# Optimization experiments

Measured on AMD Instinct MI355X. Metric: run time of the kernel, lower is better.

Reference implementation:

```python
import jax, jax.numpy as jnp
import numpy as np

B, L, D = 1, 2048, 2048
H, KVH, HD = 16, 4, 128
E, TOPK, G, TKG = 16, 4, 4, 2   # experts, top_k, n_group, topk_group
I, SH_I = 1024, 2048            # moe_intermediate, shared intermediate (1024*2)
EPS = 1e-5
THETA = 1e6
SCALE = HD ** -0.5
RSF = 2.5                        # routed_scaling_factor


def rms(x, w):
    return x * jax.lax.rsqrt(jnp.mean(x * x, axis=-1, keepdims=True) + EPS) * w


def rope(x):
    # x: [B, n_heads, L, HD], non-traditional (split-half) RoPE
    pos = jnp.arange(x.shape[2], dtype=jnp.float32)
    inv = 1.0 / (THETA ** (jnp.arange(0, HD, 2, dtype=jnp.float32) / HD))
    ang = pos[:, None] * inv[None, :]                    # [L, HD/2]
    cos, sin = jnp.cos(ang), jnp.sin(ang)
    x1, x2 = x[..., : HD // 2], x[..., HD // 2 :]
    return jnp.concatenate([x1 * cos - x2 * sin, x2 * cos + x1 * sin], axis=-1)


def setup_inputs() -> dict:
    key = jax.random.key(0)
    ks = jax.random.split(key, 13)
    s = 0.02
    mk = lambda k, shp: jax.random.normal(k, shp, jnp.float32) * s
    return {
        'x': jax.random.normal(ks[0], (B, L, D), jnp.float32),
        'w_q': mk(ks[1], (H * HD, D)),
        'w_k': mk(ks[2], (KVH * HD, D)),
        'w_v': mk(ks[3], (KVH * HD, D)),
        'w_o': mk(ks[4], (D, H * HD)),
        'q_norm_w': jnp.ones(HD, jnp.float32),
        'k_norm_w': jnp.ones(HD, jnp.float32),
        'ln1_w': jnp.ones(D, jnp.float32),
        'ln2_w': jnp.ones(D, jnp.float32),
        'gate_w': mk(ks[5], (E, D)),
        'gate_bias': mk(ks[6], (E,)),
        'wg': mk(ks[7], (E, I, D)),
        'wu': mk(ks[8], (E, I, D)),
        'wd': mk(ks[9], (E, D, I)),
        'sh_g': mk(ks[10], (SH_I, D)),
        'sh_u': mk(ks[11], (SH_I, D)),
        'sh_d': mk(ks[12], (D, SH_I)),
    }


def reference(x, w_q, w_k, w_v, w_o, q_norm_w, k_norm_w, ln1_w, ln2_w,
              gate_w, gate_bias, wg, wu, wd, sh_g, sh_u, sh_d):
    # ---- attention block ----
    h = rms(x, ln1_w)
    q = rms((h @ w_q.T).reshape(B, L, H, HD), q_norm_w).transpose(0, 2, 1, 3)
    k = rms((h @ w_k.T).reshape(B, L, KVH, HD), k_norm_w).transpose(0, 2, 1, 3)
    v = (h @ w_v.T).reshape(B, L, KVH, HD).transpose(0, 2, 1, 3)
    q, k = rope(q), rope(k)
    rep = H // KVH
    k = jnp.repeat(k, rep, axis=1)
    v = jnp.repeat(v, rep, axis=1)
    causal = jnp.tril(jnp.ones((L, L), bool))
    logits = jnp.einsum('bhqd,bhkd->bhqk', q, k) * SCALE
    logits = jnp.where(causal, logits, jnp.float32(-1e30))
    attn = jax.nn.softmax(logits, axis=-1)
    o = jnp.einsum('bhqk,bhkd->bhqd', attn, v).transpose(0, 2, 1, 3).reshape(B, L, H * HD)
    h1 = x + o @ w_o.T

    # ---- MoE block ----
    t = rms(h1, ln2_w).reshape(B * L, D)
    T = t.shape[0]
    # group-limited top-k gate (noaux_tc)
    sc = jax.nn.sigmoid(t @ gate_w.T)                    # [T, E] original scores
    s2 = sc + gate_bias
    sg = s2.reshape(T, G, E // G)
    group_scores = jax.lax.top_k(sg, 2)[0].sum(-1)       # [T, G]
    gidx = jax.lax.top_k(group_scores, TKG)[1]           # keep TKG best groups
    gmask = jnp.zeros((T, G), jnp.float32).at[jnp.arange(T)[:, None], gidx].set(1.0)
    masked = (sg * gmask[..., None]).reshape(T, E)       # dropped groups -> 0
    inds = jax.lax.top_k(masked, TOPK)[1]                # [T, TOPK]
    w = jnp.take_along_axis(sc, inds, axis=-1)
    w = w / (w.sum(-1, keepdims=True) + 1e-20) * RSF
    # combine weights scattered into [T, E]
    C = jnp.zeros((T, E), jnp.float32).at[jnp.arange(T)[:, None], inds].add(w)
    # expert SwiGLU (dense over experts, masked combine -> identical math)
    g = jnp.einsum('td,eid->tei', t, wg)
    u = jnp.einsum('td,eid->tei', t, wu)
    hm = jax.nn.silu(g) * u                               # [T, E, I]
    y = jnp.einsum('tei,edi,te->td', hm, wd, C)
    # shared experts
    sh = (jax.nn.silu(t @ sh_g.T) * (t @ sh_u.T)) @ sh_d.T
    return h1 + (y + sh).reshape(B, L, D)
```

## Files before the change

kernel.cpp:

```cpp
#include <hip/hip_runtime.h>
#include <math.h>

#define TT 2048
#define DM 2048
#define NHD 16
#define NKV 4
#define HDIM 128
#define NI 1024
#define ATT_SCALE 0.08838834764831845f

typedef unsigned short u16;
typedef __attribute__((ext_vector_type(8))) short short8;
typedef __attribute__((ext_vector_type(4))) short short4v;
typedef __attribute__((ext_vector_type(4))) float float4v;

#define AS1 __attribute__((address_space(1)))
#define AS3 __attribute__((address_space(3)))

__device__ __forceinline__ u16 f2bf(float f) {
  union { float f; unsigned u; } v; v.f = f;
  unsigned r = v.u + 0x7fffu + ((v.u >> 16) & 1u);
  return (u16)(r >> 16);
}
__device__ __forceinline__ float bf2f(u16 h) {
  union { unsigned u; float f; } v; v.u = ((unsigned)h) << 16;
  return v.f;
}
__device__ __forceinline__ float4v mfma16(short8 a, short8 b, float4v c) {
  return __builtin_amdgcn_mfma_f32_16x16x32_bf16(a, b, c, 0, 0, 0);
}
__device__ __forceinline__ void gl_lds(const u16* g, u16* l) {
  __builtin_amdgcn_global_load_lds((const AS1 void*)g, (AS3 void*)l, 16, 0, 0);
}

__global__ void cvt_split(const float* __restrict__ s, u16* __restrict__ oh,
                          u16* __restrict__ ol, int n) {
  int i = (blockIdx.x * 256 + threadIdx.x) * 4;
  if (i >= n) return;
  float4v v = *(const float4v*)(s + i);
  short4v vh, vl;
  #pragma unroll
  for (int c = 0; c < 4; ++c) {
    u16 hb = f2bf(v[c]);
    vh[c] = (short)hb;
    vl[c] = (short)f2bf(v[c] - bf2f(hb));
  }
  *(short4v*)(oh + i) = vh;
  *(short4v*)(ol + i) = vl;
}

__global__ void cvt_plain(const float* __restrict__ s, u16* __restrict__ o, int n) {
  int i = (blockIdx.x * 256 + threadIdx.x) * 8;
  if (i >= n) return;
  float4v v0 = *(const float4v*)(s + i);
  float4v v1 = *(const float4v*)(s + i + 4);
  short8 ov;
  #pragma unroll
  for (int c = 0; c < 4; ++c) {
    ov[c] = (short)f2bf(v0[c]);
    ov[c + 4] = (short)f2bf(v1[c]);
  }
  *(short8*)(o + i) = ov;
}

__global__ void rms_kernel(const float* __restrict__ in, const float* __restrict__ w,
                           u16* oh, u16* ol, float* of, u16* ob) {
  const int row = blockIdx.x, tid = threadIdx.x;
  const int lane = tid & 63, wvi = tid >> 6;
  const float* xr = in + (long)row * DM;
  float4v a = *(const float4v*)(xr + tid * 4);
  float4v b = *(const float4v*)(xr + 1024 + tid * 4);
  float ss = a[0]*a[0] + a[1]*a[1] + a[2]*a[2] + a[3]*a[3]
           + b[0]*b[0] + b[1]*b[1] + b[2]*b[2] + b[3]*b[3];
  #pragma unroll
  for (int m = 1; m < 64; m <<= 1) ss += __shfl_xor(ss, m);
  __shared__ float red[4];
  if (lane == 0) red[wvi] = ss;
  __syncthreads();
  float tot = red[0] + red[1] + red[2] + red[3];
  float sc = 1.0f / sqrtf(tot * (1.0f / 2048.0f) + 1e-5f);
  float4v w0 = *(const float4v*)(w + tid * 4);
  float4v w1 = *(const float4v*)(w + 1024 + tid * 4);
  #pragma unroll
  for (int c = 0; c < 4; ++c) {
    float v0 = a[c] * sc * w0[c];
    float v1 = b[c] * sc * w1[c];
    long i0 = (long)row * DM + tid * 4 + c;
    long i1 = i0 + 1024;
    if (oh) {
      u16 h0 = f2bf(v0); oh[i0] = h0; ol[i0] = f2bf(v0 - bf2f(h0));
      u16 h1 = f2bf(v1); oh[i1] = h1; ol[i1] = f2bf(v1 - bf2f(h1));
    }
    if (of) { of[i0] = v0; of[i1] = v1; }
    if (ob) { ob[i0] = f2bf(v0); ob[i1] = f2bf(v1); }
  }
}

__global__ void rope_kernel(const float* __restrict__ qlin, const float* __restrict__ klin,
                            const float* __restrict__ qw, const float* __restrict__ kw,
                            u16* qh, u16* ql, u16* kh, u16* kl) {
  int rw = blockIdx.x * 4 + (threadIdx.x >> 6);
  int lane = threadIdx.x & 63;
  int t = rw / 20, hh = rw - t * 20;
  const float* src; const float* nw; u16 *dh, *dl;
  if (hh < 16) {
    long ofs = (long)t * 2048 + hh * 128;
    src = qlin + ofs; nw = qw; dh = qh + ofs; dl = ql + ofs;
  } else {
    long ofs = (long)t * 512 + (hh - 16) * 128;
    src = klin + ofs; nw = kw; dh = kh + ofs; dl = kl + ofs;
  }
  float x1 = src[lane], x2 = src[lane + 64];
  float ss = x1 * x1 + x2 * x2;
  #pragma unroll
  for (int m = 1; m < 64; m <<= 1) ss += __shfl_xor(ss, m);
  float sc = 1.0f / sqrtf(ss * (1.0f / 128.0f) + 1e-5f);
  x1 *= sc * nw[lane];
  x2 *= sc * nw[lane + 64];
  double inv = pow(1.0e6, -(double)lane * (1.0 / 64.0));
  double ang = (double)t * inv;
  float cs = (float)cos(ang), sn = (float)sin(ang);
  float o1 = x1 * cs - x2 * sn;
  float o2 = x2 * cs + x1 * sn;
  u16 hb1 = f2bf(o1); dh[lane] = hb1;      dl[lane] = f2bf(o1 - bf2f(hb1));
  u16 hb2 = f2bf(o2); dh[lane + 64] = hb2; dl[lane + 64] = f2bf(o2 - bf2f(hb2));
}

struct GemmP {
  const u16* Ah; long aloOff;
  const u16* B0h; const u16* B1h; long blo0; long blo1; long bstride; int ns0;
  int K;
  const int* permA; const int* cnt; const int* offs;
  int fixedM; int maxRow;
  float* oF; int ldF;
  float* oF2; int ldF2; int osplit;
  u16* oB; long oBlo; int ldB;
  const float* addX;
  const u16* dslots; const int* inv;
};

template<int EPI, bool SPLIT>
__launch_bounds__(256, 2)
__global__ void gemm_bt(GemmP p) {
  const int e = blockIdx.z;
  const int cnt = p.cnt ? p.cnt[e] : p.fixedM;
  const int mt0 = blockIdx.x * 128;
  if (mt0 >= cnt) return;
  const int off = p.offs ? p.offs[e] : 0;
  const int nt0 = blockIdx.y * 128;

  __shared__ u16 lAh[128 * 64];
  __shared__ u16 lBh[128 * 64];
  __shared__ u16 lAl[SPLIT ? 128 * 64 : 8];
  __shared__ u16 lBl[SPLIT ? 128 * 64 : 8];

  const int tid = threadIdx.x;
  const int lane = tid & 63, wvi = tid >> 6;
  const int quad = lane >> 4, l16 = lane & 15;
  const int wm = (wvi >> 1) * 64, wn = (wvi & 1) * 64;
  const int srow = tid >> 3;
  const int scc = (tid & 7) ^ (srow & 7);

  const u16* agp[4];
  #pragma unroll
  for (int i = 0; i < 4; ++i) {
    int m = mt0 + i * 32 + srow;
    int r = off + m; if (r > p.maxRow) r = p.maxRow;
    if (p.permA) r = p.permA[r];
    agp[i] = p.Ah + (long)r * p.K + scc * 8;
  }
  const u16* bgph[4]; const u16* bgpl[4];
  #pragma unroll
  for (int j = 0; j < 4; ++j) {
    int n = nt0 + j * 32 + srow;
    const u16* bp; long lo;
    if (n < p.ns0) { bp = p.B0h + (long)e * p.bstride + (long)n * p.K; lo = p.blo0; }
    else           { bp = p.B1h + (long)e * p.bstride + (long)(n - p.ns0) * p.K; lo = p.blo1; }
    bgph[j] = bp + scc * 8;
    bgpl[j] = bp + lo + scc * 8;
  }

  float4v acc[4][4];
  #pragma unroll
  for (int a = 0; a < 4; ++a)
    #pragma unroll
    for (int b = 0; b < 4; ++b)
      acc[a][b] = (float4v){0.f, 0.f, 0.f, 0.f};

  const int wofs = wvi * 64 * 8;

  for (int k0 = 0; k0 < p.K; k0 += 64) {
    __syncthreads();
    #pragma unroll
    for (int i = 0; i < 4; ++i) {
      gl_lds(agp[i] + k0, &lAh[i * 2048 + wofs]);
      if constexpr (SPLIT) gl_lds(agp[i] + p.aloOff + k0, &lAl[i * 2048 + wofs]);
    }
    #pragma unroll
    for (int j = 0; j < 4; ++j) {
      gl_lds(bgph[j] + k0, &lBh[j * 2048 + wofs]);
      if constexpr (SPLIT) gl_lds(bgpl[j] + k0, &lBl[j * 2048 + wofs]);
    }
    __syncthreads();
    #pragma unroll
    for (int kc = 0; kc < 2; ++kc) {
      short8 ah[4], al[4], bh[4], bl[4];
      #pragma unroll
      for (int t = 0; t < 4; ++t) {
        int m = wm + t * 16 + l16;
        int ia = (m * 8 + ((kc * 4 + quad) ^ (m & 7))) * 8;
        ah[t] = *(const short8*)&lAh[ia];
        if constexpr (SPLIT) al[t] = *(const short8*)&lAl[ia];
        int n = wn + t * 16 + l16;
        int ib = (n * 8 + ((kc * 4 + quad) ^ (n & 7))) * 8;
        bh[t] = *(const short8*)&lBh[ib];
        if constexpr (SPLIT) bl[t] = *(const short8*)&lBl[ib];
      }
      #pragma unroll
      for (int mt = 0; mt < 4; ++mt)
        #pragma unroll
        for (int nt = 0; nt < 4; ++nt) {
          acc[mt][nt] = mfma16(ah[mt], bh[nt], acc[mt][nt]);
          if constexpr (SPLIT) {
            acc[mt][nt] = mfma16(ah[mt], bl[nt], acc[mt][nt]);
            acc[mt][nt] = mfma16(al[mt], bh[nt], acc[mt][nt]);
          }
        }
    }
  }

  #pragma unroll
  for (int mt = 0; mt < 4; ++mt) {
    #pragma unroll
    for (int nt = 0; nt < 4; ++nt) {
      const int n = nt0 + wn + nt * 16 + l16;
      const int mlb = wm + mt * 16 + quad * 4;
      if constexpr (EPI == 1) {
        short4v vh, vl;
        #pragma unroll
        for (int r = 0; r < 4; ++r) {
          float v = acc[mt][nt][r];
          u16 hb = f2bf(v);
          vh[r] = (short)hb;
          vl[r] = (short)f2bf(v - bf2f(hb));
        }
        long ix = (long)n * p.ldB + (mt0 + mlb);
        *(short4v*)&p.oB[ix] = vh;
        *(short4v*)&p.oB[ix + p.oBlo] = vl;
      } else {
        #pragma unroll
        for (int r = 0; r < 4; ++r) {
          const int gm = mt0 + mlb + r;
          if (gm >= cnt) continue;
          float v = acc[mt][nt][r];
          if constexpr (EPI == 0) {
            if (n < p.osplit) p.oF[(long)gm * p.ldF + n] = v;
            else p.oF2[(long)gm * p.ldF2 + (n - p.osplit)] = v;
          } else if constexpr (EPI == 2) {
            long ix = (long)gm * p.ldF + n;
            p.oF[ix] = v + p.addX[ix];
          } else if constexpr (EPI == 3) {
            p.oB[(long)(off + gm) * p.ldB + n] = f2bf(v);
          } else if constexpr (EPI == 5) {
            long ix = (long)gm * p.ldF + n;
            const int* iv = p.inv + gm * 4;
            float s = bf2f(p.dslots[(long)iv[0] * DM + n])
                    + bf2f(p.dslots[(long)iv[1] * DM + n])
                    + bf2f(p.dslots[(long)iv[2] * DM + n])
                    + bf2f(p.dslots[(long)iv[3] * DM + n]);
            p.oF[ix] = v + p.addX[ix] + s;
          }
        }
      }
    }
  }
}

__launch_bounds__(256, 2)
__global__ void attn_kernel(const u16* __restrict__ qh, const u16* __restrict__ ql,
                            const u16* __restrict__ kh, const u16* __restrict__ kl,
                            const u16* __restrict__ vh, const u16* __restrict__ vl,
                            u16* __restrict__ oh, u16* __restrict__ ol) {
  const int head = blockIdx.x;
  const int qt = (int)gridDim.y - 1 - blockIdx.y;
  const int kvh = head >> 2;
  const int tid = threadIdx.x;
  const int lane = tid & 63, wvi = tid >> 6;
  const int quad = lane >> 4, l16 = lane & 15;

  __shared__ u16 lKh[64 * 128];
  __shared__ u16 lKl[64 * 128];
  __shared__ u16 lVh[128 * 64];
  __shared__ u16 lVl[128 * 64];

  const int qbase = qt * 128;
  short8 qfh[2][4], qfl[2][4];
  #pragma unroll
  for (int mt = 0; mt < 2; ++mt) {
    int row = qbase + wvi * 32 + mt * 16 + l16;
    const u16* ph = qh + (long)row * (NHD * HDIM) + head * HDIM + quad * 8;
    const u16* pl = ql + (long)row * (NHD * HDIM) + head * HDIM + quad * 8;
    #pragma unroll
    for (int kc = 0; kc < 4; ++kc) {
      qfh[mt][kc] = *(const short8*)(ph + kc * 32);
      qfl[mt][kc] = *(const short8*)(pl + kc * 32);
    }
  }
  float4v oacc[2][8];
  #pragma unroll
  for (int mt = 0; mt < 2; ++mt)
    #pragma unroll
    for (int dt = 0; dt < 8; ++dt)
      oacc[mt][dt] = (float4v){0.f, 0.f, 0.f, 0.f};
  float mrun[2][4], lrun[2][4];
  #pragma unroll
  for (int mt = 0; mt < 2; ++mt)
    #pragma unroll
    for (int r = 0; r < 4; ++r) { mrun[mt][r] = -INFINITY; lrun[mt][r] = 0.f; }

  const int sck = (tid & 15) ^ (tid >> 4);
  const int scv = (tid & 7) ^ ((tid >> 3) & 7);
  const int nsteps = 2 * qt + 2;

  for (int kt = 0; kt < nsteps; ++kt) {
    const int t0 = kt * 64;
    __syncthreads();
    #pragma unroll
    for (int i = 0; i < 4; ++i) {
      int krow = i * 16 + (tid >> 4);
      long kg = (long)(t0 + krow) * (NKV * HDIM) + kvh * HDIM + sck * 8;
      gl_lds(kh + kg, &lKh[(i * 256 + wvi * 64) * 8]);
      gl_lds(kl + kg, &lKl[(i * 256 + wvi * 64) * 8]);
      int vrow = i * 32 + (tid >> 3);
      long vg = (long)(kvh * HDIM + vrow) * TT + t0 + scv * 8;
      gl_lds(vh + vg, &lVh[(i * 256 + wvi * 64) * 8]);
      gl_lds(vl + vg, &lVl[(i * 256 + wvi * 64) * 8]);
    }
    __syncthreads();

    float4v s[2][4];
    #pragma unroll
    for (int mt = 0; mt < 2; ++mt)
      #pragma unroll
      for (int nt = 0; nt < 4; ++nt)
        s[mt][nt] = (float4v){0.f, 0.f, 0.f, 0.f};
    #pragma unroll
    for (int kc = 0; kc < 4; ++kc) {
      #pragma unroll
      for (int nt = 0; nt < 4; ++nt) {
        int n = nt * 16 + l16;
        int idx = (n * 16 + ((kc * 4 + quad) ^ (n & 15))) * 8;
        short8 bh = *(const short8*)&lKh[idx];
        short8 bl = *(const short8*)&lKl[idx];
        #pragma unroll
        for (int mt = 0; mt < 2; ++mt) {
          s[mt][nt] = mfma16(qfh[mt][kc], bh, s[mt][nt]);
          s[mt][nt] = mfma16(qfh[mt][kc], bl, s[mt][nt]);
          s[mt][nt] = mfma16(qfl[mt][kc], bh, s[mt][nt]);
        }
      }
    }
    const bool dg = (kt >= 2 * qt);
    #pragma unroll
    for (int mt = 0; mt < 2; ++mt)
      #pragma unroll
      for (int nt = 0; nt < 4; ++nt)
        #pragma unroll
        for (int r = 0; r < 4; ++r) {
          float v = s[mt][nt][r] * ATT_SCALE;
          if (dg) {
            int kcol = t0 + nt * 16 + l16;
            int qrow = qbase + wvi * 32 + mt * 16 + quad * 4 + r;
            if (kcol > qrow) v = -1e30f;
          }
          s[mt][nt][r] = v;
        }
    float alf[2][4];
    #pragma unroll
    for (int mt = 0; mt < 2; ++mt)
      #pragma unroll
      for (int r = 0; r < 4; ++r) {
        float mx = fmaxf(fmaxf(s[mt][0][r], s[mt][1][r]), fmaxf(s[mt][2][r], s[mt][3][r]));
        mx = fmaxf(mx, __shfl_xor(mx, 1));
        mx = fmaxf(mx, __shfl_xor(mx, 2));
        mx = fmaxf(mx, __shfl_xor(mx, 4));
        mx = fmaxf(mx, __shfl_xor(mx, 8));
        float mnew = fmaxf(mrun[mt][r], mx);
        float al = expf(mrun[mt][r] - mnew);
        float ps = 0.f;
        #pragma unroll
        for (int nt = 0; nt < 4; ++nt) {
          float pv = expf(s[mt][nt][r] - mnew);
          s[mt][nt][r] = pv;
          ps += pv;
        }
        ps += __shfl_xor(ps, 1); ps += __shfl_xor(ps, 2);
        ps += __shfl_xor(ps, 4); ps += __shfl_xor(ps, 8);
        lrun[mt][r] = lrun[mt][r] * al + ps;
        mrun[mt][r] = mnew;
        alf[mt][r] = al;
      }
    #pragma unroll
    for (int mt = 0; mt < 2; ++mt)
      #pragma unroll
      for (int dt = 0; dt < 8; ++dt)
        #pragma unroll
        for (int r = 0; r < 4; ++r)
          oacc[mt][dt][r] *= alf[mt][r];
    __syncthreads();
    #pragma unroll
    for (int mt = 0; mt < 2; ++mt)
      #pragma unroll
      for (int nt = 0; nt < 4; ++nt)
        #pragma unroll
        for (int r = 0; r < 4; ++r) {
          int row = wvi * 32 + mt * 16 + quad * 4 + r;
          int col = nt * 16 + l16;
          int idx = (row * 8 + ((col >> 3) ^ (row & 7))) * 8 + (col & 7);
          float pv = s[mt][nt][r];
          u16 hb = f2bf(pv);
          lKh[idx] = hb;
          lKl[idx] = f2bf(pv - bf2f(hb));
        }
    __syncthreads();
    #pragma unroll
    for (int kc = 0; kc < 2; ++kc) {
      short8 ph[2], pl[2];
      #pragma unroll
      for (int mt = 0; mt < 2; ++mt) {
        int m = wvi * 32 + mt * 16 + l16;
        int idx = (m * 8 + ((kc * 4 + quad) ^ (m & 7))) * 8;
        ph[mt] = *(const short8*)&lKh[idx];
        pl[mt] = *(const short8*)&lKl[idx];
      }
      #pragma unroll
      for (int dt = 0; dt < 8; ++dt) {
        int d = dt * 16 + l16;
        int idx = (d * 8 + ((kc * 4 + quad) ^ (d & 7))) * 8;
        short8 wh = *(const short8*)&lVh[idx];
        short8 wl = *(const short8*)&lVl[idx];
        #pragma unroll
        for (int mt = 0; mt < 2; ++mt) {
          oacc[mt][dt] = mfma16(ph[mt], wh, oacc[mt][dt]);
          oacc[mt][dt] = mfma16(ph[mt], wl, oacc[mt][dt]);
          oacc[mt][dt] = mfma16(pl[mt], wh, oacc[mt][dt]);
        }
      }
    }
  }
  #pragma unroll
  for (int mt = 0; mt < 2; ++mt)
    #pragma unroll
    for (int dt = 0; dt < 8; ++dt)
      #pragma unroll
      for (int r = 0; r < 4; ++r) {
        int row = qbase + wvi * 32 + mt * 16 + quad * 4 + r;
        int d = dt * 16 + l16;
        float v = oacc[mt][dt][r] / lrun[mt][r];
        long ix = (long)row * (NHD * HDIM) + head * HDIM + d;
        u16 hb = f2bf(v);
        oh[ix] = hb;
        ol[ix] = f2bf(v - bf2f(hb));
      }
}

__global__ void routing_kernel(const float* __restrict__ t32, const float* __restrict__ gw,
                               const float* __restrict__ gb,
                               int* inds, float* wv, int* counts) {
  int t = blockIdx.x;
  int lane = threadIdx.x;
  const float* tr = t32 + (long)t * DM;
  float4v tv[8];
  #pragma unroll
  for (int j = 0; j < 8; ++j) tv[j] = *(const float4v*)(tr + lane * 32 + j * 4);
  float sc[16];
  for (int e = 0; e < 16; ++e) {
    const float* g = gw + (long)e * DM + lane * 32;
    float acc = 0.f;
    #pragma unroll
    for (int j = 0; j < 8; ++j) {
      float4v gv = *(const float4v*)(g + j * 4);
      acc += tv[j][0]*gv[0] + tv[j][1]*gv[1] + tv[j][2]*gv[2] + tv[j][3]*gv[3];
    }
    #pragma unroll
    for (int m = 1; m < 64; m <<= 1) acc += __shfl_xor(acc, m);
    sc[e] = 1.f / (1.f + expf(-acc));
  }
  if (lane == 0) {
    float s2[16];
    for (int e = 0; e < 16; ++e) s2[e] = sc[e] + gb[e];
    float gs[4];
    for (int g = 0; g < 4; ++g) {
      float xq[4] = { s2[4*g], s2[4*g+1], s2[4*g+2], s2[4*g+3] };
      int am = 0; float m1 = xq[0];
      for (int i = 1; i < 4; ++i) if (xq[i] > m1) { m1 = xq[i]; am = i; }
      float m2 = -1e30f;
      for (int i = 0; i < 4; ++i) if (i != am) m2 = fmaxf(m2, xq[i]);
      gs[g] = m1 + m2;
    }
    int g0 = 0;
    for (int g = 1; g < 4; ++g) if (gs[g] > gs[g0]) g0 = g;
    int g1 = -1;
    for (int g = 0; g < 4; ++g) if (g != g0 && (g1 < 0 || gs[g] > gs[g1])) g1 = g;
    float msk[16];
    for (int e = 0; e < 16; ++e) {
      int g = e >> 2;
      msk[e] = (g == g0 || g == g1) ? s2[e] : 0.0f;
    }
    int id[4]; float w[4]; float wsum = 0.f;
    for (int j = 0; j < 4; ++j) {
      int bi = 0; float bv = msk[0];
      for (int e = 1; e < 16; ++e) if (msk[e] > bv) { bv = msk[e]; bi = e; }
      id[j] = bi; w[j] = sc[bi]; msk[bi] = -1e30f;
      wsum += w[j];
    }
    float scale = 2.5f / (wsum + 1e-20f);
    for (int j = 0; j < 4; ++j) {
      inds[t * 4 + j] = id[j];
      wv[t * 4 + j] = w[j] * scale;
      atomicAdd(&counts[id[j]], 1);
    }
  }
}

__global__ void scan_kernel(int* ctrl) {
  if (threadIdx.x == 0) {
    int a = 0;
    for (int e = 0; e < 16; ++e) { ctrl[16 + e] = a; a += ctrl[e]; }
  }
}

__global__ void assign_kernel(const int* inds, const float* wv, int* ctrl,
                              int* perm, float* wslot, int* inv) {
  int t = blockIdx.x * 256 + threadIdx.x;
  if (t >= TT) return;
  for (int j = 0; j < 4; ++j) {
    int e = inds[t * 4 + j];
    int pos = atomicAdd(&ctrl[32 + e], 1);
    int s = ctrl[16 + e] + pos;
    perm[s] = t;
    wslot[s] = wv[t * 4 + j];
    inv[t * 4 + j] = s;
  }
}

__global__ void hm_moe_kernel(const u16* __restrict__ gu, const float* __restrict__ wslot,
                              u16* __restrict__ hm) {
  int slot = blockIdx.x;
  int i = threadIdx.x * 4;
  float w = wslot[slot];
  const u16* gp = gu + (long)slot * 2048;
  short4v gv = *(const short4v*)(gp + i);
  short4v uv = *(const short4v*)(gp + 1024 + i);
  short4v ov;
  #pragma unroll
  for (int c = 0; c < 4; ++c) {
    float g = bf2f((u16)gv[c]);
    float u = bf2f((u16)uv[c]);
    float h = g / (1.f + expf(-g)) * u * w;
    ov[c] = (short)f2bf(h);
  }
  *(short4v*)&hm[(long)slot * 1024 + i] = ov;
}

__global__ void hm_sh_kernel(const u16* __restrict__ gu, u16* __restrict__ hm) {
  int t = blockIdx.x;
  int i = threadIdx.x * 8;
  const u16* gp = gu + (long)t * 4096 + i;
  const u16* up = gu + (long)t * 4096 + 2048 + i;
  u16* op = hm + (long)t * 2048 + i;
  #pragma unroll
  for (int c = 0; c < 2; ++c) {
    short4v gv = *(const short4v*)(gp + c * 4);
    short4v uv = *(const short4v*)(up + c * 4);
    short4v ov;
    #pragma unroll
    for (int q = 0; q < 4; ++q) {
      float g = bf2f((u16)gv[q]);
      float u = bf2f((u16)uv[q]);
      float h = g / (1.f + expf(-g)) * u;
      ov[q] = (short)f2bf(h);
    }
    *(short4v*)(op + c * 4) = ov;
  }
}

extern "C" void kernel_launch(void* const* d_in, const int* in_sizes, int n_in,
                              void* d_out, int out_size, void* d_ws, size_t ws_size,
                              hipStream_t stream) {
  (void)in_sizes; (void)n_in; (void)out_size; (void)ws_size;
  const float* x   = (const float*)d_in[0];
  const float* wq  = (const float*)d_in[1];
  const float* wk  = (const float*)d_in[2];
  const float* wvv = (const float*)d_in[3];
  const float* wo  = (const float*)d_in[4];
  const float* qnw = (const float*)d_in[5];
  const float* knw = (const float*)d_in[6];
  const float* ln1 = (const float*)d_in[7];
  const float* ln2 = (const float*)d_in[8];
  const float* gw  = (const float*)d_in[9];
  const float* gb  = (const float*)d_in[10];
  const float* wg  = (const float*)d_in[11];
  const float* wu  = (const float*)d_in[12];
  const float* wd  = (const float*)d_in[13];
  const float* shg = (const float*)d_in[14];
  const float* shu = (const float*)d_in[15];
  const float* shd = (const float*)d_in[16];
  float* out = (float*)d_out;

  char* wp = (char*)d_ws;
  auto alloc = [&](size_t b) -> char* { char* r = wp; wp += (b + 255) & ~(size_t)255; return r; };
  u16* h_hi   = (u16*)alloc((size_t)TT * DM * 2);
  u16* h_lo   = (u16*)alloc((size_t)TT * DM * 2);
  float* q_lin = (float*)alloc((size_t)TT * 2048 * 4);
  float* k_lin = (float*)alloc((size_t)TT * 512 * 4);
  u16* q_hi   = (u16*)alloc((size_t)TT * 2048 * 2);
  u16* q_lo   = (u16*)alloc((size_t)TT * 2048 * 2);
  u16* k_hi   = (u16*)alloc((size_t)TT * 512 * 2);
  u16* k_lo   = (u16*)alloc((size_t)TT * 512 * 2);
  u16* vT_hi  = (u16*)alloc((size_t)512 * TT * 2);
  u16* vT_lo  = (u16*)alloc((size_t)512 * TT * 2);
  u16* o_hi   = (u16*)alloc((size_t)TT * 2048 * 2);
  u16* o_lo   = (u16*)alloc((size_t)TT * 2048 * 2);
  float* h1   = (float*)alloc((size_t)TT * DM * 4);
  float* t32  = (float*)alloc((size_t)TT * DM * 4);
  u16* t_bf   = (u16*)alloc((size_t)TT * DM * 2);
  u16* gu_sh  = (u16*)alloc((size_t)TT * 4096 * 2);
  u16* hm_sh  = (u16*)alloc((size_t)TT * 2048 * 2);
  u16* gu_moe = (u16*)alloc((size_t)8192 * 2048 * 2);
  u16* hm_moe = (u16*)alloc((size_t)8192 * 1024 * 2);
  u16* dtmp   = (u16*)alloc((size_t)8192 * 2048 * 2);
  int* inds   = (int*)alloc((size_t)TT * 4 * 4);
  float* wvals = (float*)alloc((size_t)TT * 4 * 4);
  int* ctrl   = (int*)alloc(256);
  int* perm   = (int*)alloc(8192 * 4);
  float* wslot = (float*)alloc(8192 * 4);
  int* inv    = (int*)alloc((size_t)TT * 4 * 4);
  const int NQ = 2048 * 2048, NK = 512 * 2048;
  u16* wq_c  = (u16*)alloc((size_t)NQ * 2 * 2);
  u16* wk_c  = (u16*)alloc((size_t)NK * 2 * 2);
  u16* wv_c  = (u16*)alloc((size_t)NK * 2 * 2);
  u16* wo_c  = (u16*)alloc((size_t)NQ * 2 * 2);
  const int NGU = 16 * NI * DM;
  u16* wg_c  = (u16*)alloc((size_t)NGU * 2);
  u16* wu_c  = (u16*)alloc((size_t)NGU * 2);
  u16* wd_c  = (u16*)alloc((size_t)NGU * 2);
  u16* shg_c = (u16*)alloc((size_t)NQ * 2);
  u16* shu_c = (u16*)alloc((size_t)NQ * 2);
  u16* shd_c = (u16*)alloc((size_t)NQ * 2);

  hipMemsetAsync(ctrl, 0, 256, stream);

  cvt_split<<<NQ / 4 / 256, 256, 0, stream>>>(wq, wq_c, wq_c + NQ, NQ);
  cvt_split<<<NK / 4 / 256, 256, 0, stream>>>(wk, wk_c, wk_c + NK, NK);
  cvt_split<<<NK / 4 / 256, 256, 0, stream>>>(wvv, wv_c, wv_c + NK, NK);
  cvt_split<<<NQ / 4 / 256, 256, 0, stream>>>(wo, wo_c, wo_c + NQ, NQ);
  cvt_plain<<<NGU / 8 / 256, 256, 0, stream>>>(wg, wg_c, NGU);
  cvt_plain<<<NGU / 8 / 256, 256, 0, stream>>>(wu, wu_c, NGU);
  cvt_plain<<<NGU / 8 / 256, 256, 0, stream>>>(wd, wd_c, NGU);
  cvt_plain<<<NQ / 8 / 256, 256, 0, stream>>>(shg, shg_c, NQ);
  cvt_plain<<<NQ / 8 / 256, 256, 0, stream>>>(shu, shu_c, NQ);
  cvt_plain<<<NQ / 8 / 256, 256, 0, stream>>>(shd, shd_c, NQ);

  rms_kernel<<<TT, 256, 0, stream>>>(x, ln1, h_hi, h_lo, nullptr, nullptr);

  { GemmP p{}; p.Ah = h_hi; p.aloOff = h_lo - h_hi;
    p.B0h = wq_c; p.blo0 = NQ; p.B1h = wk_c; p.blo1 = NK; p.ns0 = 2048;
    p.K = DM; p.fixedM = TT; p.maxRow = TT - 1;
    p.oF = q_lin; p.ldF = 2048; p.oF2 = k_lin; p.ldF2 = 512; p.osplit = 2048;
    gemm_bt<0, true><<<dim3(16, 20, 1), 256, 0, stream>>>(p); }

  { GemmP p{}; p.Ah = h_hi; p.aloOff = h_lo - h_hi;
    p.B0h = wv_c; p.blo0 = NK; p.B1h = wv_c; p.blo1 = NK; p.ns0 = 1 << 30;
    p.K = DM; p.fixedM = TT; p.maxRow = TT - 1;
    p.oB = vT_hi; p.oBlo = vT_lo - vT_hi; p.ldB = TT;
    gemm_bt<1, true><<<dim3(16, 4, 1), 256, 0, stream>>>(p); }

  rope_kernel<<<TT * 20 / 4, 256, 0, stream>>>(q_lin, k_lin, qnw, knw, q_hi, q_lo, k_hi, k_lo);

  attn_kernel<<<dim3(NHD, 16, 1), 256, 0, stream>>>(q_hi, q_lo, k_hi, k_lo, vT_hi, vT_lo, o_hi, o_lo);

  { GemmP p{}; p.Ah = o_hi; p.aloOff = o_lo - o_hi;
    p.B0h = wo_c; p.blo0 = NQ; p.B1h = wo_c; p.blo1 = NQ; p.ns0 = 1 << 30;
    p.K = DM; p.fixedM = TT; p.maxRow = TT - 1;
    p.oF = h1; p.ldF = 2048; p.addX = x;
    gemm_bt<2, true><<<dim3(16, 16, 1), 256, 0, stream>>>(p); }

  rms_kernel<<<TT, 256, 0, stream>>>(h1, ln2, nullptr, nullptr, t32, t_bf);

  routing_kernel<<<TT, 64, 0, stream>>>(t32, gw, gb, inds, wvals, ctrl);
  scan_kernel<<<1, 64, 0, stream>>>(ctrl);
  assign_kernel<<<8, 256, 0, stream>>>(inds, wvals, ctrl, perm, wslot, inv);

  { GemmP p{}; p.Ah = t_bf; p.B0h = shg_c; p.B1h = shu_c; p.ns0 = 2048; p.K = DM;
    p.fixedM = TT; p.maxRow = TT - 1; p.oB = gu_sh; p.ldB = 4096;
    gemm_bt<3, false><<<dim3(16, 32, 1), 256, 0, stream>>>(p); }
  hm_sh_kernel<<<TT, 256, 0, stream>>>(gu_sh, hm_sh);

  { GemmP p{}; p.Ah = t_bf; p.permA = perm; p.cnt = ctrl; p.offs = ctrl + 16;
    p.fixedM = TT; p.maxRow = 8191;
    p.B0h = wg_c; p.B1h = wu_c; p.ns0 = 1024; p.bstride = (long)NI * DM; p.K = DM;
    p.oB = gu_moe; p.ldB = 2048;
    gemm_bt<3, false><<<dim3(16, 16, 16), 256, 0, stream>>>(p); }
  hm_moe_kernel<<<8192, 256, 0, stream>>>(gu_moe, wslot, hm_moe);
  { GemmP p{}; p.Ah = hm_moe; p.cnt = ctrl; p.offs = ctrl + 16;
    p.fixedM = TT; p.maxRow = 8191;
    p.B0h = wd_c; p.B1h = wd_c; p.ns0 = 1 << 30; p.bstride = (long)DM * NI; p.K = NI;
    p.oB = dtmp; p.ldB = 2048;
    gemm_bt<3, false><<<dim3(16, 16, 16), 256, 0, stream>>>(p); }

  { GemmP p{}; p.Ah = hm_sh; p.B0h = shd_c; p.B1h = shd_c; p.ns0 = 1 << 30; p.K = DM;
    p.fixedM = TT; p.maxRow = TT - 1;
    p.oF = out; p.ldF = 2048; p.addX = h1; p.dslots = dtmp; p.inv = inv;
    gemm_bt<5, false><<<dim3(16, 16, 1), 256, 0, stream>>>(p); }
}
```

Baseline: 1.729 ms.

## Load K/V fragments directly from global memory and use per-wave P buffers

The attention kernel stops staging K and V tiles into shared memory with block-wide barriers. Each wave now reads its MFMA B-operands for K and V straight from global memory, relying on L1/L2 caching. The P tile gets a private shared-memory slice per wave, so all __syncthreads in the loop are removed. The cost is that each wave fetches K/V on its own, which means redundant global and cache traffic and exposed load latency without staging, in exchange for no barriers and lower LDS use.

```diff
diff --git a/kernel.cpp b/kernel.cpp
--- a/kernel.cpp
+++ b/kernel.cpp
@@ -288,10 +288,9 @@
   const int lane = tid & 63, wvi = tid >> 6;
   const int quad = lane >> 4, l16 = lane & 15;
 
-  __shared__ u16 lKh[64 * 128];
-  __shared__ u16 lKl[64 * 128];
-  __shared__ u16 lVh[128 * 64];
-  __shared__ u16 lVl[128 * 64];
+  __shared__ u16 lP[4][2][32 * 64];
+  u16* Ph = &lP[wvi][0][0];
+  u16* Pl = &lP[wvi][1][0];
 
   const int qbase = qt * 128;
   short8 qfh[2][4], qfl[2][4];
@@ -318,25 +317,12 @@
     #pragma unroll
     for (int r = 0; r < 4; ++r) { mrun[mt][r] = -INFINITY; lrun[mt][r] = 0.f; }
 
-  const int sck = (tid & 15) ^ (tid >> 4);
-  const int scv = (tid & 7) ^ ((tid >> 3) & 7);
+  const long kdiff = kl - kh;
+  const long vdiff = vl - vh;
   const int nsteps = 2 * qt + 2;
 
   for (int kt = 0; kt < nsteps; ++kt) {
     const int t0 = kt * 64;
-    __syncthreads();
-    #pragma unroll
-    for (int i = 0; i < 4; ++i) {
-      int krow = i * 16 + (tid >> 4);
-      long kg = (long)(t0 + krow) * (NKV * HDIM) + kvh * HDIM + sck * 8;
-      gl_lds(kh + kg, &lKh[(i * 256 + wvi * 64) * 8]);
-      gl_lds(kl + kg, &lKl[(i * 256 + wvi * 64) * 8]);
-      int vrow = i * 32 + (tid >> 3);
-      long vg = (long)(kvh * HDIM + vrow) * TT + t0 + scv * 8;
-      gl_lds(vh + vg, &lVh[(i * 256 + wvi * 64) * 8]);
-      gl_lds(vl + vg, &lVl[(i * 256 + wvi * 64) * 8]);
-    }
-    __syncthreads();
 
     float4v s[2][4];
     #pragma unroll
@@ -345,13 +331,13 @@
       for (int nt = 0; nt < 4; ++nt)
         s[mt][nt] = (float4v){0.f, 0.f, 0.f, 0.f};
     #pragma unroll
-    for (int kc = 0; kc < 4; ++kc) {
-      #pragma unroll
-      for (int nt = 0; nt < 4; ++nt) {
-        int n = nt * 16 + l16;
-        int idx = (n * 16 + ((kc * 4 + quad) ^ (n & 15))) * 8;
-        short8 bh = *(const short8*)&lKh[idx];
-        short8 bl = *(const short8*)&lKl[idx];
+    for (int nt = 0; nt < 4; ++nt) {
+      const u16* krow = kh + (long)(t0 + nt * 16 + l16) * (NKV * HDIM)
+                           + kvh * HDIM + quad * 8;
+      #pragma unroll
+      for (int kc = 0; kc < 4; ++kc) {
+        short8 bh = *(const short8*)(krow + kc * 32);
+        short8 bl = *(const short8*)(krow + kdiff + kc * 32);
         #pragma unroll
         for (int mt = 0; mt < 2; ++mt) {
           s[mt][nt] = mfma16(qfh[mt][kc], bh, s[mt][nt]);
@@ -360,6 +346,7 @@
         }
       }
     }
+
     const bool dg = (kt >= 2 * qt);
     #pragma unroll
     for (int mt = 0; mt < 2; ++mt)
@@ -375,6 +362,7 @@
           }
           s[mt][nt][r] = v;
         }
+
     float alf[2][4];
     #pragma unroll
     for (int mt = 0; mt < 2; ++mt)
@@ -407,38 +395,38 @@
         #pragma unroll
         for (int r = 0; r < 4; ++r)
           oacc[mt][dt][r] *= alf[mt][r];
-    __syncthreads();
+
     #pragma unroll
     for (int mt = 0; mt < 2; ++mt)
       #pragma unroll
       for (int nt = 0; nt < 4; ++nt)
         #pragma unroll
         for (int r = 0; r < 4; ++r) {
-          int row = wvi * 32 + mt * 16 + quad * 4 + r;
+          int row = mt * 16 + quad * 4 + r;
           int col = nt * 16 + l16;
           int idx = (row * 8 + ((col >> 3) ^ (row & 7))) * 8 + (col & 7);
           float pv = s[mt][nt][r];
           u16 hb = f2bf(pv);
-          lKh[idx] = hb;
-          lKl[idx] = f2bf(pv - bf2f(hb));
+          Ph[idx] = hb;
+          Pl[idx] = f2bf(pv - bf2f(hb));
         }
-    __syncthreads();
+
     #pragma unroll
     for (int kc = 0; kc < 2; ++kc) {
       short8 ph[2], pl[2];
       #pragma unroll
       for (int mt = 0; mt < 2; ++mt) {
-        int m = wvi * 32 + mt * 16 + l16;
+        int m = mt * 16 + l16;
         int idx = (m * 8 + ((kc * 4 + quad) ^ (m & 7))) * 8;
-        ph[mt] = *(const short8*)&lKh[idx];
-        pl[mt] = *(const short8*)&lKl[idx];
+        ph[mt] = *(const short8*)&Ph[idx];
+        pl[mt] = *(const short8*)&Pl[idx];
       }
       #pragma unroll
       for (int dt = 0; dt < 8; ++dt) {
-        int d = dt * 16 + l16;
-        int idx = (d * 8 + ((kc * 4 + quad) ^ (d & 7))) * 8;
-        short8 wh = *(const short8*)&lVh[idx];
-        short8 wl = *(const short8*)&lVl[idx];
+        const u16* vrow = vh + (long)(kvh * HDIM + dt * 16 + l16) * TT
+                             + t0 + kc * 32 + quad * 8;
+        short8 wh = *(const short8*)vrow;
+        short8 wl = *(const short8*)(vrow + vdiff);
         #pragma unroll
         for (int mt = 0; mt < 2; ++mt) {
           oacc[mt][dt] = mfma16(ph[mt], wh, oacc[mt][dt]);
```

Result: slower. 1.930 ms (+11.7%).

## Halve attention query tile to 64 rows and give each wave private P buffer

Applied to the files above, without the earlier changes.

The attention kernel now processes 64 query rows per block (16 per wave) instead of 128, doubling the grid to 32 query tiles per head. This gives finer causal work granularity and more blocks for occupancy. Each wave writes its softmax probabilities to its own LDS region rather than reusing the K buffer, which removes two block-wide barriers per KV step. The cost is that K/V tiles are loaded from global memory twice as often per query row, and LDS use per block grows.

```diff
diff --git a/kernel.cpp b/kernel.cpp
--- a/kernel.cpp
+++ b/kernel.cpp
@@ -282,7 +282,7 @@
                             const u16* __restrict__ vh, const u16* __restrict__ vl,
                             u16* __restrict__ oh, u16* __restrict__ ol) {
   const int head = blockIdx.x;
-  const int qt = (int)gridDim.y - 1 - blockIdx.y;
+  const int qt = 31 - (int)blockIdx.y;
   const int kvh = head >> 2;
   const int tid = threadIdx.x;
   const int lane = tid & 63, wvi = tid >> 6;
@@ -292,35 +292,33 @@
   __shared__ u16 lKl[64 * 128];
   __shared__ u16 lVh[128 * 64];
   __shared__ u16 lVl[128 * 64];
-
-  const int qbase = qt * 128;
-  short8 qfh[2][4], qfl[2][4];
-  #pragma unroll
-  for (int mt = 0; mt < 2; ++mt) {
-    int row = qbase + wvi * 32 + mt * 16 + l16;
+  __shared__ u16 lP[4][2][16 * 64];
+  u16* Ph = &lP[wvi][0][0];
+  u16* Pl = &lP[wvi][1][0];
+
+  const int qbase = qt * 64;
+  const int qrow0 = qbase + wvi * 16;
+  short8 qfh[4], qfl[4];
+  {
+    int row = qrow0 + l16;
     const u16* ph = qh + (long)row * (NHD * HDIM) + head * HDIM + quad * 8;
     const u16* pl = ql + (long)row * (NHD * HDIM) + head * HDIM + quad * 8;
     #pragma unroll
     for (int kc = 0; kc < 4; ++kc) {
-      qfh[mt][kc] = *(const short8*)(ph + kc * 32);
-      qfl[mt][kc] = *(const short8*)(pl + kc * 32);
-    }
-  }
-  float4v oacc[2][8];
-  #pragma unroll
-  for (int mt = 0; mt < 2; ++mt)
-    #pragma unroll
-    for (int dt = 0; dt < 8; ++dt)
-      oacc[mt][dt] = (float4v){0.f, 0.f, 0.f, 0.f};
-  float mrun[2][4], lrun[2][4];
-  #pragma unroll
-  for (int mt = 0; mt < 2; ++mt)
-    #pragma unroll
-    for (int r = 0; r < 4; ++r) { mrun[mt][r] = -INFINITY; lrun[mt][r] = 0.f; }
+      qfh[kc] = *(const short8*)(ph + kc * 32);
+      qfl[kc] = *(const short8*)(pl + kc * 32);
+    }
+  }
+  float4v oacc[8];
+  #pragma unroll
+  for (int dt = 0; dt < 8; ++dt) oacc[dt] = (float4v){0.f, 0.f, 0.f, 0.f};
+  float mrun[4], lrun[4];
+  #pragma unroll
+  for (int r = 0; r < 4; ++r) { mrun[r] = -INFINITY; lrun[r] = 0.f; }
 
   const int sck = (tid & 15) ^ (tid >> 4);
   const int scv = (tid & 7) ^ ((tid >> 3) & 7);
-  const int nsteps = 2 * qt + 2;
+  const int nsteps = qt + 1;
 
   for (int kt = 0; kt < nsteps; ++kt) {
     const int t0 = kt * 64;
@@ -338,12 +336,9 @@
     }
     __syncthreads();
 
-    float4v s[2][4];
-    #pragma unroll
-    for (int mt = 0; mt < 2; ++mt)
-      #pragma unroll
-      for (int nt = 0; nt < 4; ++nt)
-        s[mt][nt] = (float4v){0.f, 0.f, 0.f, 0.f};
+    float4v s[4];
+    #pragma unroll
+    for (int nt = 0; nt < 4; ++nt) s[nt] = (float4v){0.f, 0.f, 0.f, 0.f};
     #pragma unroll
     for (int kc = 0; kc < 4; ++kc) {
       #pragma unroll
@@ -352,116 +347,98 @@
         int idx = (n * 16 + ((kc * 4 + quad) ^ (n & 15))) * 8;
         short8 bh = *(const short8*)&lKh[idx];
         short8 bl = *(const short8*)&lKl[idx];
-        #pragma unroll
-        for (int mt = 0; mt < 2; ++mt) {
-          s[mt][nt] = mfma16(qfh[mt][kc], bh, s[mt][nt]);
-          s[mt][nt] = mfma16(qfh[mt][kc], bl, s[mt][nt]);
-          s[mt][nt] = mfma16(qfl[mt][kc], bh, s[mt][nt]);
+        s[nt] = mfma16(qfh[kc], bh, s[nt]);
+        s[nt] = mfma16(qfh[kc], bl, s[nt]);
+        s[nt] = mfma16(qfl[kc], bh, s[nt]);
+      }
+    }
+
+    const bool dg = (kt == qt);
+    #pragma unroll
+    for (int nt = 0; nt < 4; ++nt)
+      #pragma unroll
+      for (int r = 0; r < 4; ++r) {
+        float v = s[nt][r] * ATT_SCALE;
+        if (dg) {
+          int kcol = t0 + nt * 16 + l16;
+          int qrow = qrow0 + quad * 4 + r;
+          if (kcol > qrow) v = -1e30f;
         }
+        s[nt][r] = v;
       }
-    }
-    const bool dg = (kt >= 2 * qt);
-    #pragma unroll
-    for (int mt = 0; mt < 2; ++mt)
-      #pragma unroll
-      for (int nt = 0; nt < 4; ++nt)
-        #pragma unroll
-        for (int r = 0; r < 4; ++r) {
-          float v = s[mt][nt][r] * ATT_SCALE;
-          if (dg) {
-            int kcol = t0 + nt * 16 + l16;
-            int qrow = qbase + wvi * 32 + mt * 16 + quad * 4 + r;
-            if (kcol > qrow) v = -1e30f;
-          }
-          s[mt][nt][r] = v;
-        }
-    float alf[2][4];
-    #pragma unroll
-    for (int mt = 0; mt < 2; ++mt)
+
+    float alf[4];
+    #pragma unroll
+    for (int r = 0; r < 4; ++r) {
+      float mx = fmaxf(fmaxf(s[0][r], s[1][r]), fmaxf(s[2][r], s[3][r]));
+      mx = fmaxf(mx, __shfl_xor(mx, 1));
+      mx = fmaxf(mx, __shfl_xor(mx, 2));
+      mx = fmaxf(mx, __shfl_xor(mx, 4));
+      mx = fmaxf(mx, __shfl_xor(mx, 8));
+      float mnew = fmaxf(mrun[r], mx);
+      float al = expf(mrun[r] - mnew);
+      float ps = 0.f;
+      #pragma unroll
+      for (int nt = 0; nt < 4; ++nt) {
+        float pv = expf(s[nt][r] - mnew);
+        s[nt][r] = pv;
+        ps += pv;
+      }
+      ps += __shfl_xor(ps, 1); ps += __shfl_xor(ps, 2);
+      ps += __shfl_xor(ps, 4); ps += __shfl_xor(ps, 8);
+      lrun[r] = lrun[r] * al + ps;
+      mrun[r] = mnew;
+      alf[r] = al;
+    }
+    #pragma unroll
+    for (int dt = 0; dt < 8; ++dt)
+      #pragma unroll
+      for (int r = 0; r < 4; ++r)
+        oacc[dt][r] *= alf[r];
+
+    #pragma unroll
+    for (int nt = 0; nt < 4; ++nt)
       #pragma unroll
       for (int r = 0; r < 4; ++r) {
-        float mx = fmaxf(fmaxf(s[mt][0][r], s[mt][1][r]), fmaxf(s[mt][2][r], s[mt][3][r]));
-        mx = fmaxf(mx, __shfl_xor(mx, 1));
-        mx = fmaxf(mx, __shfl_xor(mx, 2));
-        mx = fmaxf(mx, __shfl_xor(mx, 4));
-        mx = fmaxf(mx, __shfl_xor(mx, 8));
-        float mnew = fmaxf(mrun[mt][r], mx);
-        float al = expf(mrun[mt][r] - mnew);
-        float ps = 0.f;
-        #pragma unroll
-        for (int nt = 0; nt < 4; ++nt) {
-          float pv = expf(s[mt][nt][r] - mnew);
-          s[mt][nt][r] = pv;
-          ps += pv;
-        }
-        ps += __shfl_xor(ps, 1); ps += __shfl_xor(ps, 2);
-        ps += __shfl_xor(ps, 4); ps += __shfl_xor(ps, 8);
-        lrun[mt][r] = lrun[mt][r] * al + ps;
-        mrun[mt][r] = mnew;
-        alf[mt][r] = al;
+        int row = quad * 4 + r;
+        int col = nt * 16 + l16;
+        int idx = (row * 8 + ((col >> 3) ^ (row & 7))) * 8 + (col & 7);
+        float pv = s[nt][r];
+        u16 hb = f2bf(pv);
+        Ph[idx] = hb;
+        Pl[idx] = f2bf(pv - bf2f(hb));
       }
-    #pragma unroll
-    for (int mt = 0; mt < 2; ++mt)
-      #pragma unroll
-      for (int dt = 0; dt < 8; ++dt)
-        #pragma unroll
-        for (int r = 0; r < 4; ++r)
-          oacc[mt][dt][r] *= alf[mt][r];
-    __syncthreads();
-    #pragma unroll
-    for (int mt = 0; mt < 2; ++mt)
-      #pragma unroll
-      for (int nt = 0; nt < 4; ++nt)
-        #pragma unroll
-        for (int r = 0; r < 4; ++r) {
-          int row = wvi * 32 + mt * 16 + quad * 4 + r;
-          int col = nt * 16 + l16;
-          int idx = (row * 8 + ((col >> 3) ^ (row & 7))) * 8 + (col & 7);
-          float pv = s[mt][nt][r];
-          u16 hb = f2bf(pv);
-          lKh[idx] = hb;
-          lKl[idx] = f2bf(pv - bf2f(hb));
-        }
-    __syncthreads();
+
     #pragma unroll
     for (int kc = 0; kc < 2; ++kc) {
-      short8 ph[2], pl[2];
-      #pragma unroll
-      for (int mt = 0; mt < 2; ++mt) {
-        int m = wvi * 32 + mt * 16 + l16;
-        int idx = (m * 8 + ((kc * 4 + quad) ^ (m & 7))) * 8;
-        ph[mt] = *(const short8*)&lKh[idx];
-        pl[mt] = *(const short8*)&lKl[idx];
-      }
+      int idxp = (l16 * 8 + ((kc * 4 + quad) ^ (l16 & 7))) * 8;
+      short8 ph = *(const short8*)&Ph[idxp];
+      short8 pl = *(const short8*)&Pl[idxp];
       #pragma unroll
       for (int dt = 0; dt < 8; ++dt) {
         int d = dt * 16 + l16;
         int idx = (d * 8 + ((kc * 4 + quad) ^ (d & 7))) * 8;
         short8 wh = *(const short8*)&lVh[idx];
         short8 wl = *(const short8*)&lVl[idx];
-        #pragma unroll
-        for (int mt = 0; mt < 2; ++mt) {
-          oacc[mt][dt] = mfma16(ph[mt], wh, oacc[mt][dt]);
-          oacc[mt][dt] = mfma16(ph[mt], wl, oacc[mt][dt]);
-          oacc[mt][dt] = mfma16(pl[mt], wh, oacc[mt][dt]);
-        }
+        oacc[dt] = mfma16(ph, wh, oacc[dt]);
+        oacc[dt] = mfma16(ph, wl, oacc[dt]);
+        oacc[dt] = mfma16(pl, wh, oacc[dt]);
       }
     }
   }
-  #pragma unroll
-  for (int mt = 0; mt < 2; ++mt)
-    #pragma unroll
-    for (int dt = 0; dt < 8; ++dt)
-      #pragma unroll
-      for (int r = 0; r < 4; ++r) {
-        int row = qbase + wvi * 32 + mt * 16 + quad * 4 + r;
-        int d = dt * 16 + l16;
-        float v = oacc[mt][dt][r] / lrun[mt][r];
-        long ix = (long)row * (NHD * HDIM) + head * HDIM + d;
-        u16 hb = f2bf(v);
-        oh[ix] = hb;
-        ol[ix] = f2bf(v - bf2f(hb));
-      }
+
+  #pragma unroll
+  for (int dt = 0; dt < 8; ++dt)
+    #pragma unroll
+    for (int r = 0; r < 4; ++r) {
+      int row = qrow0 + quad * 4 + r;
+      int d = dt * 16 + l16;
+      float v = oacc[dt][r] / lrun[r];
+      long ix = (long)row * (NHD * HDIM) + head * HDIM + d;
+      u16 hb = f2bf(v);
+      oh[ix] = hb;
+      ol[ix] = f2bf(v - bf2f(hb));
+    }
 }
 
 __global__ void routing_kernel(const float* __restrict__ t32, const float* __restrict__ gw,
@@ -678,7 +655,7 @@
 
   rope_kernel<<<TT * 20 / 4, 256, 0, stream>>>(q_lin, k_lin, qnw, knw, q_hi, q_lo, k_hi, k_lo);
 
-  attn_kernel<<<dim3(NHD, 16, 1), 256, 0, stream>>>(q_hi, q_lo, k_hi, k_lo, vT_hi, vT_lo, o_hi, o_lo);
+  attn_kernel<<<dim3(NHD, 32, 1), 256, 0, stream>>>(q_hi, q_lo, k_hi, k_lo, vT_hi, vT_lo, o_hi, o_lo);
 
   { GemmP p{}; p.Ah = o_hi; p.aloOff = o_lo - o_hi;
     p.B0h = wo_c; p.blo0 = NQ; p.B1h = wo_c; p.blo1 = NQ; p.ns0 = 1 << 30;
```

After: 1.549 ms. 1.12x faster.
